# Kernel optimization log

Measured on AMD Instinct MI355X. Metric: run time of the kernel, lower is better.

## Reference

```python
import jax, jax.numpy as jnp
import numpy as np


def setup_inputs() -> dict:
    key = jax.random.key(0)
    ks = jax.random.split(key, 8)
    B, L, D, N, K = 4, 4096, 1024, 64, 4
    return {
        "x": jax.random.normal(ks[0], (B, L, D), dtype=jnp.float32),
        "conv_w": jax.random.normal(ks[1], (K, 1, D), dtype=jnp.float32) * 0.1,
        "conv_b": jnp.zeros((D,), dtype=jnp.float32),
        "Wp": jax.random.normal(ks[2], (D, 2 * N), dtype=jnp.float32) * (1.0 / np.sqrt(D)),
        "bp": jnp.zeros((2 * N,), dtype=jnp.float32),
        "Ws": jax.random.normal(ks[3], (D, N), dtype=jnp.float32) * (1.0 / np.sqrt(D)),
        "bs": jnp.zeros((N,), dtype=jnp.float32),
        "A_log": jax.random.normal(ks[4], (N,), dtype=jnp.float32) * 0.02,
        "dt_log": jax.random.normal(ks[5], (N,), dtype=jnp.float32) * 0.02,
        "Wo": jax.random.normal(ks[6], (N, D), dtype=jnp.float32) * (1.0 / np.sqrt(N)),
        "bo": jnp.zeros((D,), dtype=jnp.float32),
    }


def reference(x, conv_w, conv_b, Wp, bp, Ws, bs, A_log, dt_log, Wo, bo):
    B, L, D = x.shape
    K = conv_w.shape[0]
    N = Ws.shape[1]

    # causal depthwise conv: left-pad by K-1, sum K shifted slices (K is tiny)
    x_pad = jnp.pad(x, ((0, 0), (K - 1, 0), (0, 0)))
    conv = conv_b + sum(x_pad[:, k:k + L, :] * conv_w[k, 0] for k in range(K))

    proj = conv @ Wp + bp                     # [B, L, 2N]
    B_t = jax.nn.softplus(proj[..., :N])      # [B, L, N]
    C_t = jnp.tanh(proj[..., N:])             # [B, L, N]
    u = x @ Ws + bs                           # [B, L, N]

    A = -jax.nn.softplus(A_log)               # [N]
    dt = jax.nn.softplus(dt_log)              # [N]
    decay = 1.0 + dt * A                      # [N]

    def step(state, inputs):
        u_t, b_t, c_t = inputs                # each [B, N]
        state = decay * state + dt * b_t * u_t
        return state, c_t * state

    init = jnp.zeros((B, N), dtype=x.dtype)
    xs = tuple(jnp.swapaxes(a, 0, 1) for a in (u, B_t, C_t))  # time-major
    _, ys = jax.lax.scan(step, init, xs, unroll=4)            # [L, B, N]
    y = jnp.swapaxes(ys, 0, 1)                                # [B, L, N]
    return y @ Wo + bo                                        # [B, L, D]
```

## Files before the change

### kernel.cpp

```cpp
#include <hip/hip_runtime.h>

#define B_ 4
#define L_ 4096
#define D_ 1024
#define N_ 64

typedef _Float16 f16;
typedef __attribute__((ext_vector_type(8))) _Float16 half8;
typedef __attribute__((ext_vector_type(4))) float f32x4;

__device__ __forceinline__ float softplus_f(float x) {
    return fmaxf(x, 0.0f) + log1pf(__expf(-fabsf(x)));
}

__device__ __forceinline__ float tanh_f(float x) {
    float xc = fminf(fmaxf(x, -15.0f), 15.0f);
    float e = __expf(2.0f * xc);
    return (e - 1.0f) / (e + 1.0f);
}

__global__ __launch_bounds__(256) void k_prepw(
    const float* __restrict__ Wp, const float* __restrict__ Ws,
    const float* __restrict__ Wo, f16* __restrict__ WT, f16* __restrict__ WoT)
{
    int gid = blockIdx.x * 256 + threadIdx.x;
    if (gid < 24576) {
        int r = gid >> 7, kg = gid & 127;
        const float* src; int ncol, c;
        if (r < 128) { src = Wp; ncol = 128; c = r; }
        else         { src = Ws; ncol = 64;  c = r - 128; }
        f16 h[8];
        #pragma unroll
        for (int j = 0; j < 8; j++)
            h[j] = (f16)src[(size_t)(kg * 8 + j) * ncol + c];
        *(uint4*)&WT[(size_t)r * 1024 + kg * 8] = *(uint4*)h;
    } else {
        int g2 = gid - 24576;
        int d = g2 >> 3, ng = g2 & 7;
        f16 h[8];
        #pragma unroll
        for (int j = 0; j < 8; j++)
            h[j] = (f16)Wo[(size_t)(ng * 8 + j) * D_ + d];
        *(uint4*)&WoT[(size_t)d * 64 + ng * 8] = *(uint4*)h;
    }
}

#define XS 1040
__global__ __launch_bounds__(256) void k_frontend(
    const float* __restrict__ x, const float* __restrict__ conv_w,
    const float* __restrict__ conv_b, const f16* __restrict__ WT,
    const float* __restrict__ bp, const float* __restrict__ bs,
    const float* __restrict__ dt_log,
    f16* __restrict__ zT, f16* __restrict__ cT)
{
    __shared__ __align__(16) char smem[74880];
    f16*   xh = (f16*)smem;
    f16*   ch = (f16*)(smem + 41600);
    float* sE = (float*)smem;

    const int tid = threadIdx.x;
    const int w = tid >> 6, lane = tid & 63;
    const int r = lane & 15, q = lane >> 4;
    const int T0 = blockIdx.x * 16;
    const int bb = T0 >> 12;
    const int l0 = T0 & (L_ - 1);
    const int cw0 = w * 48;

    #pragma unroll
    for (int s = 0; s < 20; s++) {
        int idx = tid + 256 * s;
        int row = idx >> 8, g = idx & 255;
        int l = l0 + row - 4;
        float4 v = make_float4(0.f, 0.f, 0.f, 0.f);
        if (l >= 0)
            v = *(const float4*)&x[((size_t)(bb * L_ + l)) * D_ + g * 4];
        f16 h[4] = {(f16)v.x, (f16)v.y, (f16)v.z, (f16)v.w};
        *(uint2*)&xh[row * XS + g * 4] = *(uint2*)h;
    }
    __syncthreads();

    {
        const int d0 = tid * 4;
        const float4 w0 = *(const float4*)&conv_w[0 * D_ + d0];
        const float4 w1 = *(const float4*)&conv_w[1 * D_ + d0];
        const float4 w2 = *(const float4*)&conv_w[2 * D_ + d0];
        const float4 w3 = *(const float4*)&conv_w[3 * D_ + d0];
        const float4 cb = *(const float4*)&conv_b[d0];
        const float cwv[4][4] = {{w0.x,w0.y,w0.z,w0.w},{w1.x,w1.y,w1.z,w1.w},
                                 {w2.x,w2.y,w2.z,w2.w},{w3.x,w3.y,w3.z,w3.w}};
        const float cbv[4] = {cb.x, cb.y, cb.z, cb.w};
        uint2 win[4];
        win[0] = *(const uint2*)&xh[1 * XS + d0];
        win[1] = *(const uint2*)&xh[2 * XS + d0];
        win[2] = *(const uint2*)&xh[3 * XS + d0];
        #pragma unroll
        for (int t = 0; t < 16; t++) {
            win[3] = *(const uint2*)&xh[(t + 4) * XS + d0];
            const f16* x0 = (const f16*)&win[0];
            const f16* x1 = (const f16*)&win[1];
            const f16* x2 = (const f16*)&win[2];
            const f16* x3 = (const f16*)&win[3];
            f16 ho[4];
            #pragma unroll
            for (int j = 0; j < 4; j++) {
                float s = cbv[j];
                s = fmaf(cwv[0][j], (float)x0[j], s);
                s = fmaf(cwv[1][j], (float)x1[j], s);
                s = fmaf(cwv[2][j], (float)x2[j], s);
                s = fmaf(cwv[3][j], (float)x3[j], s);
                ho[j] = (f16)s;
            }
            *(uint2*)&ch[t * XS + d0] = *(uint2*)ho;
            win[0] = win[1]; win[1] = win[2]; win[2] = win[3];
        }
    }
    __syncthreads();

    f32x4 acc[3] = {};
    const bool needC = (cw0 < 128);
    const bool needR = (cw0 + 32 >= 128);
    const bool uc0 = (cw0      < 128);
    const bool uc1 = (cw0 + 16 < 128);
    const bool uc2 = (cw0 + 32 < 128);
    const int klq = q * 8;
    #pragma unroll 4
    for (int j = 0; j < 32; j++) {
        const int kk = j * 32 + klq;
        half8 a0 = *(const half8*)&WT[(size_t)(cw0 +      r) * 1024 + kk];
        half8 a1 = *(const half8*)&WT[(size_t)(cw0 + 16 + r) * 1024 + kk];
        half8 a2 = *(const half8*)&WT[(size_t)(cw0 + 32 + r) * 1024 + kk];
        half8 bc = {}, br = {};
        if (needC) bc = *(const half8*)&ch[r * XS + kk];
        if (needR) br = *(const half8*)&xh[(r + 4) * XS + kk];
        acc[0] = __builtin_amdgcn_mfma_f32_16x16x32_f16(a0, uc0 ? bc : br, acc[0], 0, 0, 0);
        acc[1] = __builtin_amdgcn_mfma_f32_16x16x32_f16(a1, uc1 ? bc : br, acc[1], 0, 0, 0);
        acc[2] = __builtin_amdgcn_mfma_f32_16x16x32_f16(a2, uc2 ? bc : br, acc[2], 0, 0, 0);
    }

    float* sB = sE;
    float* sC = sE + 16 * 68;
    float* sU = sE + 2 * 16 * 68;
    __syncthreads();
    #pragma unroll
    for (int mf = 0; mf < 3; mf++) {
        const int cb4 = cw0 + mf * 16 + q * 4;
        const int seg = cb4 >> 6;
        const int cl = cb4 & 63;
        const float4 bb4 = (seg == 2) ? *(const float4*)&bs[cl]
                                      : *(const float4*)&bp[cb4];
        float* dst = (seg == 0) ? sB : (seg == 1 ? sC : sU);
        float v0 = acc[mf][0] + bb4.x;
        float v1 = acc[mf][1] + bb4.y;
        float v2 = acc[mf][2] + bb4.z;
        float v3 = acc[mf][3] + bb4.w;
        if (seg == 0) {
            v0 = softplus_f(v0); v1 = softplus_f(v1);
            v2 = softplus_f(v2); v3 = softplus_f(v3);
        } else if (seg == 1) {
            v0 = tanh_f(v0); v1 = tanh_f(v1);
            v2 = tanh_f(v2); v3 = tanh_f(v3);
        }
        float4 vv = {v0, v1, v2, v3};
        *(float4*)&dst[r * 68 + cl] = vv;
    }
    __syncthreads();

    {
        const int n = tid >> 2, tg = tid & 3;
        const float dtv = softplus_f(dt_log[n]);
        f16 hz[4], hc[4];
        #pragma unroll
        for (int j = 0; j < 4; j++) {
            const int t = tg * 4 + j;
            hz[j] = (f16)(dtv * sB[t * 68 + n] * sU[t * 68 + n]);
            hc[j] = (f16)sC[t * 68 + n];
        }
        size_t o = ((size_t)(bb * N_ + n)) * L_ + l0 + tg * 4;
        *(uint2*)&zT[o] = *(uint2*)hz;
        *(uint2*)&cT[o] = *(uint2*)hc;
    }
}
#undef XS

#define ZI(i) ((i) + ((i) >> 4))
__global__ __launch_bounds__(256) void k_scan(
    const f16* __restrict__ zT, const f16* __restrict__ cT,
    const float* __restrict__ A_log, const float* __restrict__ dt_log,
    f16* __restrict__ yH)
{
    __shared__ float zs[4352];
    __shared__ float cs[4352];
    __shared__ float sA[4], sB[4];
    const int bn = blockIdx.x;
    const int n = bn & (N_ - 1);
    const int tid = threadIdx.x;
    const int lane = tid & 63, w = tid >> 6;
    const f16* zp = zT + (size_t)bn * L_;
    const f16* cp = cT + (size_t)bn * L_;

    #pragma unroll
    for (int it = 0; it < 2; it++) {
        int i = tid * 8 + it * 2048;
        uint4 rz = *(const uint4*)(zp + i);
        uint4 rc = *(const uint4*)(cp + i);
        const f16* hz = (const f16*)&rz;
        const f16* hc = (const f16*)&rc;
        #pragma unroll
        for (int k = 0; k < 8; k++) {
            zs[ZI(i + k)] = (float)hz[k];
            cs[ZI(i + k)] = (float)hc[k];
        }
    }
    __syncthreads();

    float dtv = softplus_f(dt_log[n]);
    float Av = -softplus_f(A_log[n]);
    float dec = fmaf(dtv, Av, 1.0f);

    const int base = tid * 17;
    float s = 0.0f;
    #pragma unroll
    for (int j = 0; j < 16; j++) s = fmaf(dec, s, zs[base + j]);

    float d2 = dec * dec, d4 = d2 * d2, d8 = d4 * d4, d16 = d8 * d8;

    float Ag = d16, Bg = s;
    #pragma unroll
    for (int off = 1; off < 64; off <<= 1) {
        float Ap = __shfl_up(Ag, off);
        float Bp = __shfl_up(Bg, off);
        if (lane >= off) { Bg = fmaf(Ag, Bp, Bg); Ag *= Ap; }
    }
    if (lane == 63) { sA[w] = Ag; sB[w] = Bg; }
    __syncthreads();

    float Bc = 0.0f;
    for (int i = 0; i < w; i++) Bc = fmaf(sA[i], Bc, sB[i]);
    float Ae = __shfl_up(Ag, 1);
    float Be = __shfl_up(Bg, 1);
    if (lane == 0) { Ae = 1.0f; Be = 0.0f; }
    float carry = fmaf(Ae, Bc, Be);

    float st = carry;
    #pragma unroll
    for (int j = 0; j < 16; j++) {
        st = fmaf(dec, st, zs[base + j]);
        zs[base + j] = cs[base + j] * st;
    }
    __syncthreads();

    f16* yp = yH + (size_t)bn * L_;
    #pragma unroll
    for (int it = 0; it < 2; it++) {
        int i = tid * 8 + it * 2048;
        f16 h[8];
        #pragma unroll
        for (int k = 0; k < 8; k++) h[k] = (f16)zs[ZI(i + k)];
        *(uint4*)&yp[i] = *(uint4*)h;
    }
}
#undef ZI

__global__ __launch_bounds__(256) void k_out(
    const f16* __restrict__ yH, const f16* __restrict__ WoT,
    const float* __restrict__ bo, float* __restrict__ out)
{
    __shared__ __align__(16) f16 ys[64 * 72];
    const int tid = threadIdx.x;
    const int w = tid >> 6, lane = tid & 63;
    const int r = lane & 15, q = lane >> 4;
    const int T0 = blockIdx.x * 64;
    const int bb = T0 >> 12, l0 = T0 & (L_ - 1);
    const int dw = blockIdx.y * 128 + w * 32;

    {
        const int n = tid & 63, tg = tid >> 6;
        #pragma unroll
        for (int h2 = 0; h2 < 2; h2++) {
            uint4 v = *(const uint4*)&yH[((size_t)(bb * N_ + n)) * L_ + l0 + tg * 16 + h2 * 8];
            const f16* hh = (const f16*)&v;
            #pragma unroll
            for (int j = 0; j < 8; j++)
                ys[(tg * 16 + h2 * 8 + j) * 72 + n] = hh[j];
        }
    }
    __syncthreads();

    f32x4 acc[2][4] = {};
    #pragma unroll
    for (int ks = 0; ks < 2; ks++) {
        const int kk = ks * 32 + q * 8;
        half8 af[2];
        #pragma unroll
        for (int mf = 0; mf < 2; mf++)
            af[mf] = *(const half8*)&WoT[(size_t)(dw + mf * 16 + r) * 64 + kk];
        #pragma unroll
        for (int nf = 0; nf < 4; nf++) {
            half8 bf = *(const half8*)&ys[(nf * 16 + r) * 72 + kk];
            #pragma unroll
            for (int mf = 0; mf < 2; mf++)
                acc[mf][nf] = __builtin_amdgcn_mfma_f32_16x16x32_f16(
                    af[mf], bf, acc[mf][nf], 0, 0, 0);
        }
    }

    #pragma unroll
    for (int mf = 0; mf < 2; mf++) {
        const int d = dw + mf * 16 + q * 4;
        const float4 bb4 = *(const float4*)&bo[d];
        #pragma unroll
        for (int nf = 0; nf < 4; nf++) {
            const int t = T0 + nf * 16 + r;
            float4 o = {acc[mf][nf][0] + bb4.x, acc[mf][nf][1] + bb4.y,
                        acc[mf][nf][2] + bb4.z, acc[mf][nf][3] + bb4.w};
            *(float4*)&out[(size_t)t * D_ + d] = o;
        }
    }
}

extern "C" void kernel_launch(void* const* d_in, const int* in_sizes, int n_in,
                              void* d_out, int out_size, void* d_ws, size_t ws_size,
                              hipStream_t stream) {
    const float* x      = (const float*)d_in[0];
    const float* conv_w = (const float*)d_in[1];
    const float* conv_b = (const float*)d_in[2];
    const float* Wp     = (const float*)d_in[3];
    const float* bp     = (const float*)d_in[4];
    const float* Ws     = (const float*)d_in[5];
    const float* bs     = (const float*)d_in[6];
    const float* A_log  = (const float*)d_in[7];
    const float* dt_log = (const float*)d_in[8];
    const float* Wo     = (const float*)d_in[9];
    const float* bo     = (const float*)d_in[10];
    float* out = (float*)d_out;

    char* wsp = (char*)d_ws;
    f16* WT  = (f16*)wsp;
    f16* WoT = (f16*)(wsp + 393216);
    f16* zT  = (f16*)(wsp + 524288);
    f16* cT  = (f16*)(wsp + 2621440);
    f16* yH  = (f16*)(wsp + 4718592);

    k_prepw<<<dim3(128), dim3(256), 0, stream>>>(Wp, Ws, Wo, WT, WoT);
    k_frontend<<<dim3(B_ * L_ / 16), dim3(256), 0, stream>>>(
        x, conv_w, conv_b, WT, bp, bs, dt_log, zT, cT);
    k_scan<<<dim3(B_ * N_), dim3(256), 0, stream>>>(zT, cT, A_log, dt_log, yH);
    k_out<<<dim3(B_ * L_ / 64, D_ / 128), dim3(256), 0, stream>>>(yH, WoT, bo, out);
}
```

Baseline: 200.8 us.

## Restructure frontend into 64-token tiles with double-buffered K-chunked weight staging

The frontend kernel now processes 64 tokens per 512-thread block instead of 16 per 256-thread block. It walks the 1024-wide reduction in 64-column chunks, staging the fused weight slice into XOR-swizzled shared memory and prefetching the next chunk's weights and inputs into registers while the current chunk's convolution and MFMAs run. Weight reads from global memory drop roughly fourfold per token, and the shared-memory footprint shrinks enough for two blocks per CU. It also coalesces the prepw weight-transpose reads. The cost is a more complex pipeline with two barriers per chunk and higher register pressure.

```diff
diff --git a/kernel.cpp b/kernel.cpp
--- a/kernel.cpp
+++ b/kernel.cpp
@@ -17,6 +17,12 @@
     float xc = fminf(fmaxf(x, -15.0f), 15.0f);
     float e = __expf(2.0f * xc);
     return (e - 1.0f) / (e + 1.0f);
+}
+
+__device__ __forceinline__ void bar_raw() {
+    asm volatile("" ::: "memory");
+    __builtin_amdgcn_s_barrier();
+    asm volatile("" ::: "memory");
 }
 
 __global__ __launch_bounds__(256) void k_prepw(
@@ -24,19 +30,24 @@
     const float* __restrict__ Wo, f16* __restrict__ WT, f16* __restrict__ WoT)
 {
     int gid = blockIdx.x * 256 + threadIdx.x;
-    if (gid < 24576) {
-        int r = gid >> 7, kg = gid & 127;
-        const float* src; int ncol, c;
-        if (r < 128) { src = Wp; ncol = 128; c = r; }
-        else         { src = Ws; ncol = 64;  c = r - 128; }
+    if (gid < 16384) {
+        int c = gid & 127, kg = gid >> 7;
         f16 h[8];
         #pragma unroll
         for (int j = 0; j < 8; j++)
-            h[j] = (f16)src[(size_t)(kg * 8 + j) * ncol + c];
-        *(uint4*)&WT[(size_t)r * 1024 + kg * 8] = *(uint4*)h;
+            h[j] = (f16)Wp[(size_t)(kg * 8 + j) * 128 + c];
+        *(uint4*)&WT[(size_t)c * 1024 + kg * 8] = *(uint4*)h;
+    } else if (gid < 24576) {
+        int idx = gid - 16384;
+        int c = idx & 63, kg = idx >> 6;
+        f16 h[8];
+        #pragma unroll
+        for (int j = 0; j < 8; j++)
+            h[j] = (f16)Ws[(size_t)(kg * 8 + j) * 64 + c];
+        *(uint4*)&WT[(size_t)(128 + c) * 1024 + kg * 8] = *(uint4*)h;
     } else {
-        int g2 = gid - 24576;
-        int d = g2 >> 3, ng = g2 & 7;
+        int idx = gid - 24576;
+        int d = idx & 1023, ng = idx >> 10;
         f16 h[8];
         #pragma unroll
         for (int j = 0; j < 8; j++)
@@ -45,142 +56,177 @@
     }
 }
 
-#define XS 1040
-__global__ __launch_bounds__(256) void k_frontend(
+__global__ __launch_bounds__(512, 2) void k_frontend(
     const float* __restrict__ x, const float* __restrict__ conv_w,
     const float* __restrict__ conv_b, const f16* __restrict__ WT,
     const float* __restrict__ bp, const float* __restrict__ bs,
     const float* __restrict__ dt_log,
     f16* __restrict__ zT, f16* __restrict__ cT)
 {
-    __shared__ __align__(16) char smem[74880];
-    f16*   xh = (f16*)smem;
-    f16*   ch = (f16*)(smem + 41600);
+    __shared__ __align__(16) char smem[65536];
+    char* wt0 = smem;
+    char* wt1 = smem + 24576;
+    char* chb = smem + 49152;
+    char* xhb = smem + 57344;
     float* sE = (float*)smem;
 
     const int tid = threadIdx.x;
     const int w = tid >> 6, lane = tid & 63;
     const int r = lane & 15, q = lane >> 4;
-    const int T0 = blockIdx.x * 16;
-    const int bb = T0 >> 12;
-    const int l0 = T0 & (L_ - 1);
-    const int cw0 = w * 48;
-
-    #pragma unroll
-    for (int s = 0; s < 20; s++) {
-        int idx = tid + 256 * s;
-        int row = idx >> 8, g = idx & 255;
-        int l = l0 + row - 4;
-        float4 v = make_float4(0.f, 0.f, 0.f, 0.f);
-        if (l >= 0)
-            v = *(const float4*)&x[((size_t)(bb * L_ + l)) * D_ + g * 4];
-        f16 h[4] = {(f16)v.x, (f16)v.y, (f16)v.z, (f16)v.w};
-        *(uint2*)&xh[row * XS + g * 4] = *(uint2*)h;
-    }
-    __syncthreads();
-
-    {
-        const int d0 = tid * 4;
-        const float4 w0 = *(const float4*)&conv_w[0 * D_ + d0];
-        const float4 w1 = *(const float4*)&conv_w[1 * D_ + d0];
-        const float4 w2 = *(const float4*)&conv_w[2 * D_ + d0];
-        const float4 w3 = *(const float4*)&conv_w[3 * D_ + d0];
-        const float4 cb = *(const float4*)&conv_b[d0];
-        const float cwv[4][4] = {{w0.x,w0.y,w0.z,w0.w},{w1.x,w1.y,w1.z,w1.w},
-                                 {w2.x,w2.y,w2.z,w2.w},{w3.x,w3.y,w3.z,w3.w}};
-        const float cbv[4] = {cb.x, cb.y, cb.z, cb.w};
-        uint2 win[4];
-        win[0] = *(const uint2*)&xh[1 * XS + d0];
-        win[1] = *(const uint2*)&xh[2 * XS + d0];
-        win[2] = *(const uint2*)&xh[3 * XS + d0];
-        #pragma unroll
-        for (int t = 0; t < 16; t++) {
-            win[3] = *(const uint2*)&xh[(t + 4) * XS + d0];
-            const f16* x0 = (const f16*)&win[0];
-            const f16* x1 = (const f16*)&win[1];
-            const f16* x2 = (const f16*)&win[2];
-            const f16* x3 = (const f16*)&win[3];
-            f16 ho[4];
-            #pragma unroll
-            for (int j = 0; j < 4; j++) {
-                float s = cbv[j];
-                s = fmaf(cwv[0][j], (float)x0[j], s);
-                s = fmaf(cwv[1][j], (float)x1[j], s);
-                s = fmaf(cwv[2][j], (float)x2[j], s);
-                s = fmaf(cwv[3][j], (float)x3[j], s);
-                ho[j] = (f16)s;
-            }
-            *(uint2*)&ch[t * XS + d0] = *(uint2*)ho;
-            win[0] = win[1]; win[1] = win[2]; win[2] = win[3];
-        }
-    }
-    __syncthreads();
-
-    f32x4 acc[3] = {};
-    const bool needC = (cw0 < 128);
-    const bool needR = (cw0 + 32 >= 128);
-    const bool uc0 = (cw0      < 128);
-    const bool uc1 = (cw0 + 16 < 128);
-    const bool uc2 = (cw0 + 32 < 128);
-    const int klq = q * 8;
-    #pragma unroll 4
-    for (int j = 0; j < 32; j++) {
-        const int kk = j * 32 + klq;
-        half8 a0 = *(const half8*)&WT[(size_t)(cw0 +      r) * 1024 + kk];
-        half8 a1 = *(const half8*)&WT[(size_t)(cw0 + 16 + r) * 1024 + kk];
-        half8 a2 = *(const half8*)&WT[(size_t)(cw0 + 32 + r) * 1024 + kk];
-        half8 bc = {}, br = {};
-        if (needC) bc = *(const half8*)&ch[r * XS + kk];
-        if (needR) br = *(const half8*)&xh[(r + 4) * XS + kk];
-        acc[0] = __builtin_amdgcn_mfma_f32_16x16x32_f16(a0, uc0 ? bc : br, acc[0], 0, 0, 0);
-        acc[1] = __builtin_amdgcn_mfma_f32_16x16x32_f16(a1, uc1 ? bc : br, acc[1], 0, 0, 0);
-        acc[2] = __builtin_amdgcn_mfma_f32_16x16x32_f16(a2, uc2 ? bc : br, acc[2], 0, 0, 0);
+    const int wr = w >> 2, wc = w & 3;
+    const int T0 = blockIdx.x * 64;
+    const int bb = T0 >> 12, l0 = T0 & (L_ - 1);
+    const int cbase = wc * 48;
+    const int ct0 = (tid >> 4) * 2;
+    const int cd  = (tid & 15) * 4;
+
+    f32x4 acc[3][2] = {};
+
+    #define WLOAD(RS, c) { _Pragma("unroll") \
+        for (int s = 0; s < 3; s++) { \
+            int slot = tid + 512 * s; \
+            RS[s] = *(const uint4*)&WT[(size_t)(slot >> 3) * 1024 + (c) * 64 + (slot & 7) * 8]; \
+        } }
+    #define DSWT(BUF, RS) { _Pragma("unroll") \
+        for (int s = 0; s < 3; s++) { \
+            int slot = tid + 512 * s; int row = slot >> 3, g = slot & 7; \
+            *(uint4*)((BUF) + row * 128 + ((g * 16) ^ ((row & 7) << 4))) = RS[s]; \
+        } }
+    #define XWLOAD(RX, RW, c) { _Pragma("unroll") \
+        for (int i = 0; i < 5; i++) { \
+            int l = l0 + ct0 - 3 + i; \
+            f32x4 v = {0.f, 0.f, 0.f, 0.f}; \
+            if (l >= 0) v = *(const f32x4*)&x[((size_t)(bb * L_ + l)) * D_ + (c) * 64 + cd]; \
+            RX[i] = v; } \
+        _Pragma("unroll") \
+        for (int k = 0; k < 4; k++) \
+            RW[k] = *(const f32x4*)&conv_w[k * D_ + (c) * 64 + cd]; \
+        RW[4] = *(const f32x4*)&conv_b[(c) * 64 + cd]; }
+
+    #define CONV(RX, RW) { _Pragma("unroll") \
+        for (int tt = 0; tt < 2; tt++) { \
+            const int t = ct0 + tt; \
+            f16 hc4[4], hx4[4]; \
+            _Pragma("unroll") \
+            for (int j = 0; j < 4; j++) { \
+                float s0 = RW[4][j]; \
+                s0 = fmaf(RW[0][j], RX[tt + 0][j], s0); \
+                s0 = fmaf(RW[1][j], RX[tt + 1][j], s0); \
+                s0 = fmaf(RW[2][j], RX[tt + 2][j], s0); \
+                s0 = fmaf(RW[3][j], RX[tt + 3][j], s0); \
+                hc4[j] = (f16)s0; hx4[j] = (f16)RX[tt + 3][j]; \
+            } \
+            const int cb = (cd * 2) ^ ((t & 7) << 4); \
+            *(uint2*)(chb + t * 128 + cb) = *(uint2*)hc4; \
+            *(uint2*)(xhb + t * 128 + cb) = *(uint2*)hx4; \
+        } }
+
+    #define MFMA_PH(WTC) { \
+        const bool nC = (cbase < 128); \
+        const bool nX = (cbase + 32 >= 128); \
+        _Pragma("unroll") \
+        for (int ks = 0; ks < 2; ks++) { \
+            const int cb16 = ks * 64 + q * 16; \
+            half8 a8[3]; \
+            _Pragma("unroll") \
+            for (int mf = 0; mf < 3; mf++) { \
+                const int ar = cbase + mf * 16 + r; \
+                a8[mf] = *(const half8*)((WTC) + ar * 128 + (cb16 ^ ((ar & 7) << 4))); \
+            } \
+            _Pragma("unroll") \
+            for (int nf = 0; nf < 2; nf++) { \
+                const int tr = wr * 32 + nf * 16 + r; \
+                const int tb = cb16 ^ ((tr & 7) << 4); \
+                half8 bc = {}, bx = {}; \
+                if (nC) bc = *(const half8*)(chb + tr * 128 + tb); \
+                if (nX) bx = *(const half8*)(xhb + tr * 128 + tb); \
+                acc[0][nf] = __builtin_amdgcn_mfma_f32_16x16x32_f16( \
+                    a8[0], (cbase < 128) ? bc : bx, acc[0][nf], 0, 0, 0); \
+                acc[1][nf] = __builtin_amdgcn_mfma_f32_16x16x32_f16( \
+                    a8[1], (cbase + 16 < 128) ? bc : bx, acc[1][nf], 0, 0, 0); \
+                acc[2][nf] = __builtin_amdgcn_mfma_f32_16x16x32_f16( \
+                    a8[2], (cbase + 32 < 128) ? bc : bx, acc[2][nf], 0, 0, 0); \
+            } \
+        } }
+
+    #define CHUNK(c, RX, RW, RSN, RXN, RWN, WTC, WTN, PF) { \
+        if (PF) { WLOAD(RSN, (c) + 1); XWLOAD(RXN, RWN, (c) + 1); } \
+        CONV(RX, RW); \
+        asm volatile("s_waitcnt lgkmcnt(0)" ::: "memory"); \
+        __builtin_amdgcn_sched_barrier(0); \
+        __builtin_amdgcn_s_barrier(); \
+        asm volatile("" ::: "memory"); \
+        MFMA_PH(WTC); \
+        if (PF) { DSWT(WTN, RSN); } \
+        bar_raw(); }
+
+    f32x4 rXa[5], rWa[5], rXb[5], rWb[5];
+    uint4 rSa[3], rSb[3];
+
+    WLOAD(rSa, 0);
+    XWLOAD(rXa, rWa, 0);
+    DSWT(wt0, rSa);
+    __syncthreads();
+
+    #pragma unroll 1
+    for (int cc = 0; cc < 8; cc++) {
+        const int c0 = cc * 2;
+        CHUNK(c0,     rXa, rWa, rSb, rXb, rWb, wt0, wt1, true);
+        CHUNK(c0 + 1, rXb, rWb, rSa, rXa, rWa, wt1, wt0, (c0 + 1) < 15);
     }
 
     float* sB = sE;
-    float* sC = sE + 16 * 68;
-    float* sU = sE + 2 * 16 * 68;
-    __syncthreads();
+    float* sC = sE + 64 * 68;
+    float* sU = sE + 2 * 64 * 68;
     #pragma unroll
     for (int mf = 0; mf < 3; mf++) {
-        const int cb4 = cw0 + mf * 16 + q * 4;
+        const int cb4 = cbase + mf * 16 + q * 4;
         const int seg = cb4 >> 6;
         const int cl = cb4 & 63;
         const float4 bb4 = (seg == 2) ? *(const float4*)&bs[cl]
                                       : *(const float4*)&bp[cb4];
         float* dst = (seg == 0) ? sB : (seg == 1 ? sC : sU);
-        float v0 = acc[mf][0] + bb4.x;
-        float v1 = acc[mf][1] + bb4.y;
-        float v2 = acc[mf][2] + bb4.z;
-        float v3 = acc[mf][3] + bb4.w;
-        if (seg == 0) {
-            v0 = softplus_f(v0); v1 = softplus_f(v1);
-            v2 = softplus_f(v2); v3 = softplus_f(v3);
-        } else if (seg == 1) {
-            v0 = tanh_f(v0); v1 = tanh_f(v1);
-            v2 = tanh_f(v2); v3 = tanh_f(v3);
-        }
-        float4 vv = {v0, v1, v2, v3};
-        *(float4*)&dst[r * 68 + cl] = vv;
+        #pragma unroll
+        for (int nf = 0; nf < 2; nf++) {
+            const int t = wr * 32 + nf * 16 + r;
+            float v0 = acc[mf][nf][0] + bb4.x;
+            float v1 = acc[mf][nf][1] + bb4.y;
+            float v2 = acc[mf][nf][2] + bb4.z;
+            float v3 = acc[mf][nf][3] + bb4.w;
+            if (seg == 0) {
+                v0 = softplus_f(v0); v1 = softplus_f(v1);
+                v2 = softplus_f(v2); v3 = softplus_f(v3);
+            } else if (seg == 1) {
+                v0 = tanh_f(v0); v1 = tanh_f(v1);
+                v2 = tanh_f(v2); v3 = tanh_f(v3);
+            }
+            float4 vv = {v0, v1, v2, v3};
+            *(float4*)&dst[t * 68 + cl] = vv;
+        }
     }
     __syncthreads();
 
     {
-        const int n = tid >> 2, tg = tid & 3;
+        const int n = tid >> 3, tg = tid & 7;
         const float dtv = softplus_f(dt_log[n]);
-        f16 hz[4], hc[4];
-        #pragma unroll
-        for (int j = 0; j < 4; j++) {
-            const int t = tg * 4 + j;
+        f16 hz[8], hc2[8];
+        #pragma unroll
+        for (int j = 0; j < 8; j++) {
+            const int t = tg * 8 + j;
             hz[j] = (f16)(dtv * sB[t * 68 + n] * sU[t * 68 + n]);
-            hc[j] = (f16)sC[t * 68 + n];
-        }
-        size_t o = ((size_t)(bb * N_ + n)) * L_ + l0 + tg * 4;
-        *(uint2*)&zT[o] = *(uint2*)hz;
-        *(uint2*)&cT[o] = *(uint2*)hc;
-    }
-}
-#undef XS
+            hc2[j] = (f16)sC[t * 68 + n];
+        }
+        size_t o = ((size_t)(bb * N_ + n)) * L_ + l0 + tg * 8;
+        *(uint4*)&zT[o] = *(uint4*)hz;
+        *(uint4*)&cT[o] = *(uint4*)hc2;
+    }
+    #undef WLOAD
+    #undef DSWT
+    #undef XWLOAD
+    #undef CONV
+    #undef MFMA_PH
+    #undef CHUNK
+}
 
 #define ZI(i) ((i) + ((i) >> 4))
 __global__ __launch_bounds__(256) void k_scan(
@@ -342,7 +388,7 @@
     f16* yH  = (f16*)(wsp + 4718592);
 
     k_prepw<<<dim3(128), dim3(256), 0, stream>>>(Wp, Ws, Wo, WT, WoT);
-    k_frontend<<<dim3(B_ * L_ / 16), dim3(256), 0, stream>>>(
+    k_frontend<<<dim3(B_ * L_ / 64), dim3(512), 0, stream>>>(
         x, conv_w, conv_b, WT, bp, bs, dt_log, zT, cT);
     k_scan<<<dim3(B_ * N_), dim3(256), 0, stream>>>(zT, cT, A_log, dt_log, yH);
     k_out<<<dim3(B_ * L_ / 64, D_ / 128), dim3(256), 0, stream>>>(yH, WoT, bo, out);
```

Result: faster. 188.0 us (-6.4%).
